# Kernel tuning notes

Measured on AMD Instinct MI355X. Metric: run time of the kernel, lower is better.

The kernel has to match this reference:

```python
import jax, jax.numpy as jnp
import numpy as np

B, S, K, E, H = 64, 25, 20, 256, 8
D = 2 * E  # MHA embed dim (item emb concat user emb)


def setup_inputs() -> dict:
    key = jax.random.key(0)
    ks = jax.random.split(key, 10)
    def w(k, shp, scale=0.02):
        return jax.random.normal(k, shp, jnp.float32) * scale
    return dict(
        item_embs=jax.random.normal(ks[0], (B, S, K, E), jnp.float32),
        user_embs=jax.random.normal(ks[1], (B, E), jnp.float32),
        responses=jax.random.randint(ks[2], (B, S, K), 0, 2),
        Wq=w(ks[3], (D, D)), bq=jnp.zeros((D,), jnp.float32),
        Wk=w(ks[4], (D, D)), bk=jnp.zeros((D,), jnp.float32),
        Wv=w(ks[5], (D, D)), bv=jnp.zeros((D,), jnp.float32),
        Wo=w(ks[6], (D, D)), bo=jnp.zeros((D,), jnp.float32),
        ln_g=jnp.ones((D,), jnp.float32), ln_b=jnp.zeros((D,), jnp.float32),
        W1=w(ks[7], (D, D)), b1=jnp.zeros((D,), jnp.float32),
        W2=w(ks[8], (1, D)), b2=jnp.zeros((1,), jnp.float32),
    )


def _scot_forward(item_embs, user_embs, responses, Wq, bq, Wk, bk, Wv, bv,
                  Wo, bo, ln_g, ln_b, W1, b1, W2, b2):
    Bt, St, Kt, Et = item_embs.shape
    Dt = 2 * Et
    L = St * Kt + 1  # all slate items + prepended zero item
    hd = Dt // H
    # stack_embeddings: concat item emb with broadcast user emb -> [B,S,K,2E]
    x = jnp.concatenate(
        [item_embs, jnp.broadcast_to(user_embs[:, None, None, :], (Bt, St, Kt, Et))], -1)
    x = x.reshape(Bt, St * Kt, Dt)
    # add_zero_item: prepend an all-zero token (slate number 0)
    x = jnp.concatenate([jnp.zeros((Bt, 1, Dt), x.dtype), x], axis=1)  # [B,L,D]
    # slate number per token: 0 for zero item, then 1..S repeated slate_size times
    slateno = jnp.concatenate(
        [jnp.zeros((1,), jnp.int32),
         jnp.repeat(jnp.arange(1, St + 1, dtype=jnp.int32), Kt)])  # [L]
    # clicked mask (zero item counts as clicked) -> keys visible to attention
    clicked = jnp.concatenate(
        [jnp.ones((Bt, 1), bool), responses.reshape(Bt, St * Kt) > 0], axis=1)  # [B,L]
    # attn_mask in the original blocks slateno_q <= slateno_k, except column 0;
    # combined with key_padding over non-clicked keys this equals:
    base_allow = slateno[:, None] > slateno[None, :]
    base_allow = base_allow.at[:, 0].set(True)            # zero item always visible
    allow = base_allow[None, :, :] & clicked[:, None, :]  # [B,L,L]
    # torch MultiheadAttention (batch_first)
    def heads(h):
        return h.reshape(Bt, L, H, hd).transpose(0, 2, 1, 3)  # [B,H,L,hd]
    q = heads(x @ Wq.T + bq)
    k = heads(x @ Wk.T + bk)
    v = heads(x @ Wv.T + bv)
    scores = jnp.einsum('bhqd,bhkd->bhqk', q, k) / np.sqrt(hd).astype(np.float32)
    scores = jnp.where(allow[:, None, :, :], scores, -jnp.inf)
    attn = jax.nn.softmax(scores, axis=-1)
    f = jnp.einsum('bhqk,bhkd->bhqd', attn, v)
    f = f.transpose(0, 2, 1, 3).reshape(Bt, L, Dt) @ Wo.T + bo
    f = f[:, 1:, :]  # drop zero-item query
    # out head: LayerNorm -> Linear -> GELU(exact) -> Linear
    mu = f.mean(-1, keepdims=True)
    var = ((f - mu) ** 2).mean(-1, keepdims=True)
    f = (f - mu) / jnp.sqrt(var + 1e-5) * ln_g + ln_b
    h = jax.nn.gelu(f @ W1.T + b1, approximate=False)
    out = h @ W2.T + b2  # [B, S*K, 1]
    return out.reshape(Bt, St, Kt)


def reference(item_embs, user_embs, responses, Wq, bq, Wk, bk, Wv, bv,
              Wo, bo, ln_g, ln_b, W1, b1, W2, b2):
    return _scot_forward(item_embs, user_embs, responses, Wq, bq, Wk, bk,
                         Wv, bv, Wo, bo, ln_g, ln_b, W1, b1, W2, b2)
```

## Files before the change

### kernel.cpp

```cpp
#include <hip/hip_runtime.h>
#include <math.h>

#define BATCH 64
#define SLATES 25
#define KPS 20
#define EDIM 256
#define DDIM 512
#define HEADS 8
#define HD 64
#define LFULL 501
#define NROWS 500
#define MTOT (BATCH*NROWS)
#define CMAX 512
#define NQKV 1536
#define RB 32
#define NRB ((NROWS + RB - 1) / RB)

typedef __attribute__((ext_vector_type(8))) short short8;
typedef __attribute__((ext_vector_type(4))) float f32x4;

__device__ __forceinline__ unsigned short f2bf(float x) {
    unsigned int u = __builtin_bit_cast(unsigned int, x);
    u = (u + 0x7FFFu + ((u >> 16) & 1u)) >> 16;
    return (unsigned short)u;
}
__device__ __forceinline__ float bf2f(unsigned short s) {
    unsigned int u = ((unsigned int)s) << 16;
    return __builtin_bit_cast(float, u);
}
__device__ __forceinline__ float gelu_exact(float x) {
    return 0.5f * x * (1.0f + erff(x * 0.70710678118654752440f));
}
__device__ __forceinline__ void gload16(const void* g, void* l) {
    __builtin_amdgcn_global_load_lds(
        (const __attribute__((address_space(1))) void*)g,
        (__attribute__((address_space(3))) void*)l, 16, 0, 0);
}

__global__ __launch_bounds__(256) void cvt_kernel(
    const float* __restrict__ src, unsigned short* __restrict__ dst, int n4)
{
    const int i = blockIdx.x * 256 + threadIdx.x;
    if (i >= n4) return;
    float4 v = ((const float4*)src)[i];
    ushort4 o;
    o.x = f2bf(v.x); o.y = f2bf(v.y); o.z = f2bf(v.z); o.w = f2bf(v.w);
    ((ushort4*)dst)[i] = o;
}

__global__ __launch_bounds__(256) void packqkv_kernel(
    const float* __restrict__ Wq, const float* __restrict__ Wk,
    const float* __restrict__ Wv, unsigned short* __restrict__ dst)
{
    const int y = blockIdx.y;
    const float* W = (y == 0) ? Wq : (y == 1) ? Wk : Wv;
    const int i = blockIdx.x * 256 + threadIdx.x;
    const int row = i >> 6, c4 = (i & 63) * 4;
    float4 v = *(const float4*)&W[(size_t)row * DDIM + c4];
    ushort4 o;
    o.x = f2bf(v.x); o.y = f2bf(v.y); o.z = f2bf(v.z); o.w = f2bf(v.w);
    *(ushort4*)&dst[((size_t)y * DDIM + row) * EDIM + c4] = o;
}

__global__ __launch_bounds__(256) void w1prep_kernel(
    const float* __restrict__ W1, const float* __restrict__ g,
    const float* __restrict__ lnb, unsigned short* __restrict__ W1g,
    float2* __restrict__ c1c2)
{
    const int row = blockIdx.x * 4 + (threadIdx.x >> 6);
    const int lane = threadIdx.x & 63;
    float c1 = 0.f, c2 = 0.f;
#pragma unroll
    for (int i = 0; i < 8; ++i) {
        const int k = lane + i * 64;
        const float w = W1[(size_t)row * DDIM + k];
        const float gv = g[k];
        c1 += w * lnb[k];
        c2 += w * gv;
        W1g[(size_t)row * DDIM + k] = f2bf(w * gv);
    }
#pragma unroll
    for (int off = 32; off; off >>= 1) {
        c1 += __shfl_xor(c1, off, 64);
        c2 += __shfl_xor(c2, off, 64);
    }
    if (lane == 0) c1c2[row] = make_float2(c1, c2);
}

__global__ __launch_bounds__(64) void compact_kernel(
    const int* __restrict__ resp, int* __restrict__ cidx, int* __restrict__ cnt)
{
    const int b = blockIdx.x, lane = threadIdx.x;
    int a[8]; int c = 0;
#pragma unroll
    for (int j = 0; j < 8; ++j) {
        const int l = lane * 8 + j;
        int al = 0;
        if (l == 0) al = 1;
        else if (l <= NROWS) al = (resp[(size_t)b * NROWS + l - 1] > 0) ? 1 : 0;
        a[j] = al; c += al;
    }
    int incl = c;
#pragma unroll
    for (int off = 1; off < 64; off <<= 1) {
        int t = __shfl_up(incl, off, 64);
        if (lane >= off) incl += t;
    }
    int run = incl - c;
#pragma unroll
    for (int j = 0; j < 8; ++j) {
        const int l = lane * 8 + j;
        if (l >= 1 && l <= 481 && (l % 20) == 1)
            cnt[b * 32 + (l - 1) / 20] = run;
        cidx[b * 512 + l] = a[j] ? run : -1;
        run += a[j];
    }
}

__global__ __launch_bounds__(256) void user_bias_kernel(
    const float* __restrict__ user,
    const float* __restrict__ Wq, const float* __restrict__ bq,
    const float* __restrict__ Wk, const float* __restrict__ bk,
    const float* __restrict__ Wv, const float* __restrict__ bv,
    float* __restrict__ uball,
    unsigned short* __restrict__ qb, unsigned short* __restrict__ kc,
    unsigned short* __restrict__ vc)
{
    const int b = blockIdx.x;
    const int y = blockIdx.y;
    const int tid = threadIdx.x;
    const float* W  = (y == 0) ? Wq : (y == 1) ? Wk : Wv;
    const float* bi = (y == 0) ? bq : (y == 1) ? bk : bv;

    __shared__ float us[EDIM];
    if (tid < EDIM) us[tid] = user[b * EDIM + tid];
    __syncthreads();
    for (int o = tid; o < DDIM; o += 256) {
        float s = bi[o];
        const float* wr = &W[(size_t)o * DDIM + EDIM];
#pragma unroll 4
        for (int e = 0; e < EDIM; ++e) s += us[e] * wr[e];
        uball[(size_t)b * NQKV + y * DDIM + o] = s;
        const int hh = o >> 6, dd = o & 63;
        const size_t bh = (size_t)b * HEADS + hh;
        if (y == 0)      qb[(bh * LFULL) * HD + dd] = f2bf(bi[o]);
        else if (y == 1) kc[(bh * CMAX) * HD + dd] = f2bf(bi[o]);
        else             vc[(bh * HD + dd) * CMAX] = f2bf(bi[o]);
    }
}

__global__ __launch_bounds__(256) void gemm_qkv(
    const unsigned short* __restrict__ A,
    const unsigned short* __restrict__ Wqkv,
    const float* __restrict__ uball, const int* __restrict__ cidx,
    unsigned short* __restrict__ oq, unsigned short* __restrict__ ok,
    unsigned short* __restrict__ ov)
{
    const int tid = threadIdx.x;
    const int lin = blockIdx.y * gridDim.x + blockIdx.x;
    const int vb  = (lin & 7) * 375 + (lin >> 3);
    const int n0 = (vb % 12) * 128;
    const int m0 = (vb / 12) * 128;
    const int lane = tid & 63, wid = tid >> 6;
    const int wm = (wid & 1) * 64, wn = (wid >> 1) * 64;

    __shared__ __align__(16) unsigned short sm[24576];
    __shared__ int cids[128];
    auto As = [&](int buf) { return (unsigned short(*)[32])(sm + buf * 4096); };
    auto Ws = [&](int buf) { return (unsigned short(*)[32])(sm + 12288 + buf * 4096); };
    auto bounce = (unsigned short(*)[136])sm;

    f32x4 acc[4][4];
#pragma unroll
    for (int i = 0; i < 4; ++i)
#pragma unroll
        for (int j = 0; j < 4; ++j) acc[i][j] = (f32x4){0.f, 0.f, 0.f, 0.f};

    const unsigned short* gA0 = &A[(size_t)(m0 + wid * 16 + (lane >> 2)) * EDIM + (lane & 3) * 8];
    const unsigned short* gA1 = gA0 + (size_t)64 * EDIM;
    const unsigned short* gW0 = &Wqkv[(size_t)(n0 + wid * 16 + (lane >> 2)) * EDIM + (lane & 3) * 8];
    const unsigned short* gW1 = gW0 + (size_t)64 * EDIM;
    const int frow = lane & 15, fk = (lane >> 4) * 8;

    auto stage = [&](int buf, int k0) {
        gload16(gA0 + k0, &As(buf)[wid * 16][0]);
        gload16(gA1 + k0, &As(buf)[64 + wid * 16][0]);
        gload16(gW0 + k0, &Ws(buf)[wid * 16][0]);
        gload16(gW1 + k0, &Ws(buf)[64 + wid * 16][0]);
    };
    stage(0, 0);
    stage(1, 32);

    const int nst = EDIM / 32;
    for (int t = 0; t < nst; ++t) {
        const int cur = t % 3;
        if (t < nst - 1) asm volatile("s_waitcnt vmcnt(4)" ::: "memory");
        else             asm volatile("s_waitcnt vmcnt(0)" ::: "memory");
        __builtin_amdgcn_s_barrier();
        __builtin_amdgcn_sched_barrier(0);
        short8 af[4], wf[4];
#pragma unroll
        for (int mi = 0; mi < 4; ++mi)
            af[mi] = *(const short8*)&As(cur)[wm + mi * 16 + frow][fk];
#pragma unroll
        for (int ni = 0; ni < 4; ++ni)
            wf[ni] = *(const short8*)&Ws(cur)[wn + ni * 16 + frow][fk];
#pragma unroll
        for (int mi = 0; mi < 4; ++mi)
#pragma unroll
            for (int ni = 0; ni < 4; ++ni)
                acc[mi][ni] = __builtin_amdgcn_mfma_f32_16x16x32_bf16(
                    af[mi], wf[ni], acc[mi][ni], 0, 0, 0);
        if (t + 2 < nst) stage((t + 2) % 3, (t + 2) * 32);
    }

    const int z = n0 >> 9;
    const int b0 = m0 / NROWS;
    const int split = (b0 + 1) * NROWS;
    const int b1 = (split <= m0 + 127) ? b0 + 1 : b0;
    float ub0[4], ub1[4];
#pragma unroll
    for (int ni = 0; ni < 4; ++ni) {
        const int np = n0 + wn + ni * 16 + frow;
        ub0[ni] = uball[(size_t)b0 * NQKV + np];
        ub1[ni] = uball[(size_t)b1 * NQKV + np];
    }
    __syncthreads();
    if (z != 0 && tid < 128) {
        const int m = m0 + tid;
        const int b = (m >= split) ? b1 : b0;
        cids[tid] = cidx[b * 512 + (m - b * NROWS + 1)];
    }
#pragma unroll
    for (int mi = 0; mi < 4; ++mi)
#pragma unroll
        for (int r = 0; r < 4; ++r) {
            const int ml = wm + mi * 16 + (lane >> 4) * 4 + r;
            const bool hi = (m0 + ml >= split);
#pragma unroll
            for (int ni = 0; ni < 4; ++ni)
                bounce[ml][wn + ni * 16 + frow] =
                    f2bf(acc[mi][ni][r] + (hi ? ub1[ni] : ub0[ni]));
        }
    __syncthreads();

    const int h0 = (n0 & 511) >> 6;
    if (z == 0) {
        const int row = tid >> 1, half = tid & 1;
        const int m = m0 + row;
        const int b = (m >= split) ? b1 : b0;
        const int l = m - b * NROWS + 1;
        unsigned short* dst = &oq[(((size_t)b * HEADS + h0 + half) * LFULL + l) * HD];
        const unsigned short* src = &bounce[row][half * 64];
#pragma unroll
        for (int j = 0; j < 8; ++j)
            *(uint4*)(dst + j * 8) = *(const uint4*)(src + j * 8);
    } else if (z == 1) {
        const int row = tid >> 1, half = tid & 1;
        const int c = cids[row];
        if (c >= 0) {
            const int m = m0 + row;
            const int b = (m >= split) ? b1 : b0;
            unsigned short* dst = &ok[(((size_t)b * HEADS + h0 + half) * CMAX + c) * HD];
            const unsigned short* src = &bounce[row][half * 64];
#pragma unroll
            for (int j = 0; j < 8; ++j)
                *(uint4*)(dst + j * 8) = *(const uint4*)(src + j * 8);
        }
    } else {
        const int col = tid & 127, mh = tid >> 7;
        const int hh = h0 + (col >> 6), dd = col & 63;
        for (int mm = 0; mm < 64; ++mm) {
            const int row = mh * 64 + mm;
            const int c = cids[row];
            if (c >= 0) {
                const int m = m0 + row;
                const int b = (m >= split) ? b1 : b0;
                ov[((size_t)b * HEADS + hh) * (size_t)(HD * CMAX)
                   + (size_t)dd * CMAX + c] = bounce[row][col];
            }
        }
    }
}

template <int MODE>
__global__ __launch_bounds__(256) void gemm_bf16(
    const unsigned short* __restrict__ A,
    const unsigned short* __restrict__ W,
    const float* __restrict__ bias, void* __restrict__ outp,
    const float* __restrict__ W2, float* __restrict__ part,
    const float2* __restrict__ musr, const float2* __restrict__ c1c2)
{
    const int tid = threadIdx.x;
    const int lin = blockIdx.y * gridDim.x + blockIdx.x;
    const int vb  = (lin & 7) * 125 + (lin >> 3);
    const int n0 = (vb % 4) * 128;
    const int m0 = (vb / 4) * 128;
    const int lane = tid & 63, wid = tid >> 6;
    const int wm = (wid & 1) * 64, wn = (wid >> 1) * 64;

    __shared__ unsigned short As[3][128][32];
    __shared__ unsigned short Ws[3][128][32];

    f32x4 acc[4][4];
#pragma unroll
    for (int i = 0; i < 4; ++i)
#pragma unroll
        for (int j = 0; j < 4; ++j) acc[i][j] = (f32x4){0.f, 0.f, 0.f, 0.f};

    const unsigned short* gA0 = &A[(size_t)(m0 + wid * 16 + (lane >> 2)) * DDIM + (lane & 3) * 8];
    const unsigned short* gA1 = gA0 + (size_t)64 * DDIM;
    const unsigned short* gW0 = &W[(size_t)(n0 + wid * 16 + (lane >> 2)) * DDIM + (lane & 3) * 8];
    const unsigned short* gW1 = gW0 + (size_t)64 * DDIM;
    const int frow = lane & 15, fk = (lane >> 4) * 8;

    auto stage = [&](int buf, int k0) {
        gload16(gA0 + k0, &As[buf][wid * 16][0]);
        gload16(gA1 + k0, &As[buf][64 + wid * 16][0]);
        gload16(gW0 + k0, &Ws[buf][wid * 16][0]);
        gload16(gW1 + k0, &Ws[buf][64 + wid * 16][0]);
    };
    stage(0, 0);
    stage(1, 32);

    const int nst = DDIM / 32;
    for (int t = 0; t < nst; ++t) {
        const int cur = t % 3;
        if (t < nst - 1) asm volatile("s_waitcnt vmcnt(4)" ::: "memory");
        else             asm volatile("s_waitcnt vmcnt(0)" ::: "memory");
        __builtin_amdgcn_s_barrier();
        __builtin_amdgcn_sched_barrier(0);
        short8 af[4], wf[4];
#pragma unroll
        for (int mi = 0; mi < 4; ++mi)
            af[mi] = *(const short8*)&As[cur][wm + mi * 16 + frow][fk];
#pragma unroll
        for (int ni = 0; ni < 4; ++ni)
            wf[ni] = *(const short8*)&Ws[cur][wn + ni * 16 + frow][fk];
#pragma unroll
        for (int mi = 0; mi < 4; ++mi)
#pragma unroll
            for (int ni = 0; ni < 4; ++ni)
                acc[mi][ni] = __builtin_amdgcn_mfma_f32_16x16x32_bf16(
                    af[mi], wf[ni], acc[mi][ni], 0, 0, 0);
        if (t + 2 < nst) stage((t + 2) % 3, (t + 2) * 32);
    }

    const int slot = (n0 >> 7) * 2 + (wn >> 6);
    if (MODE == 1) {
        float bv4[4];
#pragma unroll
        for (int ni = 0; ni < 4; ++ni) bv4[ni] = bias[n0 + wn + ni * 16 + frow];
#pragma unroll
        for (int mi = 0; mi < 4; ++mi)
#pragma unroll
            for (int r = 0; r < 4; ++r) {
                const int m = m0 + wm + mi * 16 + (lane >> 4) * 4 + r;
                float s1 = 0.f, s2 = 0.f;
#pragma unroll
                for (int ni = 0; ni < 4; ++ni) {
                    const float v = acc[mi][ni][r] + bv4[ni];
                    s1 += v; s2 += v * v;
                    ((unsigned short*)outp)[(size_t)m * DDIM + n0 + wn + ni * 16 + frow]
                        = f2bf(v);
                }
                s1 += __shfl_xor(s1, 1, 64); s2 += __shfl_xor(s2, 1, 64);
                s1 += __shfl_xor(s1, 2, 64); s2 += __shfl_xor(s2, 2, 64);
                s1 += __shfl_xor(s1, 4, 64); s2 += __shfl_xor(s2, 4, 64);
                s1 += __shfl_xor(s1, 8, 64); s2 += __shfl_xor(s2, 8, 64);
                if (frow == 0) {
                    part[((size_t)m << 4) + slot * 2]     = s1;
                    part[((size_t)m << 4) + slot * 2 + 1] = s2;
                }
            }
    } else {
        float w2v[4], cb[4], c2v[4];
#pragma unroll
        for (int ni = 0; ni < 4; ++ni) {
            const int n = n0 + wn + ni * 16 + frow;
            w2v[ni] = W2[n];
            const float2 cc = c1c2[n];
            cb[ni]  = cc.x + bias[n];
            c2v[ni] = cc.y;
        }
#pragma unroll
        for (int mi = 0; mi < 4; ++mi)
#pragma unroll
            for (int r = 0; r < 4; ++r) {
                const int m = m0 + wm + mi * 16 + (lane >> 4) * 4 + r;
                const float2 ms = musr[m];
                float s = 0.f;
#pragma unroll
                for (int ni = 0; ni < 4; ++ni)
                    s += gelu_exact(ms.y * (acc[mi][ni][r] - ms.x * c2v[ni]) + cb[ni])
                         * w2v[ni];
                s += __shfl_xor(s, 1, 64);
                s += __shfl_xor(s, 2, 64);
                s += __shfl_xor(s, 4, 64);
                s += __shfl_xor(s, 8, 64);
                if (frow == 0)
                    part[(size_t)m * 8 + slot] = s;
            }
    }
}

__global__ __launch_bounds__(256) void lnstats_kernel(
    const float* __restrict__ rowpart, float2* __restrict__ musr)
{
    const int m = blockIdx.x * 256 + threadIdx.x;
    if (m >= MTOT) return;
    const float* p = rowpart + ((size_t)m << 4);
    float s1 = 0.f, s2 = 0.f;
#pragma unroll
    for (int i = 0; i < 8; ++i) { s1 += p[i * 2]; s2 += p[i * 2 + 1]; }
    const float mu = s1 * (1.0f / DDIM);
    const float var = s2 * (1.0f / DDIM) - mu * mu;
    musr[m] = make_float2(mu, rsqrtf(var + 1e-5f));
}

__global__ __launch_bounds__(256) void w2red_kernel(
    const float* __restrict__ part, const float* __restrict__ b2,
    float* __restrict__ out)
{
    const int m = blockIdx.x * 256 + threadIdx.x;
    if (m >= MTOT) return;
    const float* p = part + (size_t)m * 8;
    float s = b2[0];
#pragma unroll
    for (int i = 0; i < 8; ++i) s += p[i];
    out[m] = s;
}

__global__ __launch_bounds__(256) void attn_mfma(
    const unsigned short* __restrict__ qx, const unsigned short* __restrict__ kc,
    const unsigned short* __restrict__ vc, const int* __restrict__ cnt,
    unsigned short* __restrict__ outb)
{
    const int lin = blockIdx.x + NRB * (blockIdx.y + HEADS * blockIdx.z);
    const int vbk = (lin & 7) * (NRB * HEADS * BATCH / 8) + (lin >> 3);
    const int rbk = vbk % NRB;
    const int h   = (vbk / NRB) % HEADS;
    const int b   = vbk / (NRB * HEADS);
    const int g0  = rbk * RB;

    const int tid = threadIdx.x, lane = tid & 63, w = tid >> 6;

    __shared__ __align__(16) unsigned short scb[RB][520];
    __shared__ float rsw[4][RB];
    __shared__ int snck[RB];

    const int frow = lane & 15, fk = (lane >> 4) * 8;
    const size_t bh = (size_t)b * HEADS + h;
    const unsigned short* kbase = kc + bh * (CMAX * HD);
    const unsigned short* vbase = vc + bh * (HD * CMAX);

    if (tid < RB) {
        const int s = (g0 + tid >= NROWS ? NROWS - 1 : g0 + tid) / KPS;
        snck[tid] = cnt[b * 32 + s];
    }

    short8 qf[2][2];
#pragma unroll
    for (int mi = 0; mi < 2; ++mi) {
        const int qrow = g0 + mi * 16 + frow;
#pragma unroll
        for (int ks = 0; ks < 2; ++ks) {
            short8 v = {};
            if (qrow < NROWS)
                v = *(const short8*)&qx[(bh * LFULL + qrow + 1) * HD + ks * 32 + fk];
            qf[mi][ks] = v;
        }
    }
    __syncthreads();

    int nck8[2][4];
#pragma unroll
    for (int mi = 0; mi < 2; ++mi)
#pragma unroll
        for (int r = 0; r < 4; ++r)
            nck8[mi][r] = snck[mi * 16 + (lane >> 4) * 4 + r];
    const int nmax = snck[RB - 1];
    const int NT = (nmax + 63) >> 6;

    f32x4 rsum[2];
    rsum[0] = (f32x4){0.f, 0.f, 0.f, 0.f};
    rsum[1] = (f32x4){0.f, 0.f, 0.f, 0.f};
    for (int t = 0; t < NT; ++t) {
        const int key = (t << 6) + w * 16 + frow;
        const unsigned short* kr = kbase + (size_t)key * HD;
        const short8 kf0 = *(const short8*)(kr + fk);
        const short8 kf1 = *(const short8*)(kr + 32 + fk);
        f32x4 s2[2];
#pragma unroll
        for (int mi = 0; mi < 2; ++mi) {
            s2[mi] = (f32x4){0.f, 0.f, 0.f, 0.f};
            s2[mi] = __builtin_amdgcn_mfma_f32_16x16x32_bf16(qf[mi][0], kf0, s2[mi], 0, 0, 0);
            s2[mi] = __builtin_amdgcn_mfma_f32_16x16x32_bf16(qf[mi][1], kf1, s2[mi], 0, 0, 0);
        }
#pragma unroll
        for (int mi = 0; mi < 2; ++mi)
#pragma unroll
            for (int r = 0; r < 4; ++r) {
                const int row = mi * 16 + (lane >> 4) * 4 + r;
                const float p = (key < nck8[mi][r]) ? __expf(s2[mi][r] * 0.125f) : 0.f;
                rsum[mi][r] += p;
                scb[row][key] = f2bf(p);
            }
    }
#pragma unroll
    for (int mi = 0; mi < 2; ++mi)
#pragma unroll
        for (int r = 0; r < 4; ++r) {
            float v = rsum[mi][r];
            v += __shfl_xor(v, 1, 64);
            v += __shfl_xor(v, 2, 64);
            v += __shfl_xor(v, 4, 64);
            v += __shfl_xor(v, 8, 64);
            if (frow == 0)
                rsw[w][mi * 16 + (lane >> 4) * 4 + r] = v;
        }
    __syncthreads();

    f32x4 po[2];
    po[0] = (f32x4){0.f, 0.f, 0.f, 0.f};
    po[1] = (f32x4){0.f, 0.f, 0.f, 0.f};
    const unsigned short* vrow = vbase + (size_t)(w * 16 + frow) * CMAX;
    for (int t = 0; t < NT; ++t) {
#pragma unroll
        for (int ks = 0; ks < 2; ++ks) {
            const int kb0 = (t << 6) + ks * 32 + fk;
            const short8 vf = *(const short8*)(vrow + kb0);
#pragma unroll
            for (int mi = 0; mi < 2; ++mi) {
                const short8 pf = *(const short8*)&scb[mi * 16 + frow][kb0];
                po[mi] = __builtin_amdgcn_mfma_f32_16x16x32_bf16(pf, vf, po[mi], 0, 0, 0);
            }
        }
    }

#pragma unroll
    for (int mi = 0; mi < 2; ++mi)
#pragma unroll
        for (int r = 0; r < 4; ++r) {
            const int row = mi * 16 + (lane >> 4) * 4 + r;
            const int m = g0 + row;
            if (m < NROWS) {
                const float inv = 1.0f / (rsw[0][row] + rsw[1][row]
                                        + rsw[2][row] + rsw[3][row]);
                outb[((size_t)b * NROWS + m) * DDIM
                     + h * HD + w * 16 + frow] = f2bf(po[mi][r] * inv);
            }
        }
}

extern "C" void kernel_launch(void* const* d_in, const int* in_sizes, int n_in,
                              void* d_out, int out_size, void* d_ws, size_t ws_size,
                              hipStream_t stream)
{
    const float* item = (const float*)d_in[0];
    const float* user = (const float*)d_in[1];
    const int*   resp = (const int*)d_in[2];
    const float* Wq = (const float*)d_in[3];  const float* bq = (const float*)d_in[4];
    const float* Wk = (const float*)d_in[5];  const float* bk = (const float*)d_in[6];
    const float* Wv = (const float*)d_in[7];  const float* bv = (const float*)d_in[8];
    const float* Wo = (const float*)d_in[9];  const float* bo = (const float*)d_in[10];
    const float* lng = (const float*)d_in[11]; const float* lnb = (const float*)d_in[12];
    const float* W1 = (const float*)d_in[13]; const float* b1 = (const float*)d_in[14];
    const float* W2 = (const float*)d_in[15]; const float* b2 = (const float*)d_in[16];
    float* out = (float*)d_out;

    char* p = (char*)d_ws;
    auto alloc = [&](size_t bytes) { char* r = p; p += (bytes + 255) & ~(size_t)255; return r; };
    const size_t NITEM = (size_t)BATCH * NROWS * EDIM;
    const size_t NW    = (size_t)DDIM * DDIM;
    const size_t NQ    = (size_t)BATCH * HEADS * LFULL * HD;
    const size_t NC    = (size_t)BATCH * HEADS * CMAX * HD;
    const size_t NMD   = (size_t)MTOT * DDIM;
    const size_t PAD   = 8192;

    unsigned short* itemb  = (unsigned short*)alloc(NITEM * 2);
    unsigned short* Wqkvb  = (unsigned short*)alloc((size_t)NQKV * EDIM * 2);
    unsigned short* Wob    = (unsigned short*)alloc(NW * 2);
    unsigned short* W1gb   = (unsigned short*)alloc(NW * 2);
    unsigned short* qb     = (unsigned short*)alloc(NQ * 2 + PAD);
    unsigned short* kcb    = (unsigned short*)alloc(NC * 2 + PAD);
    unsigned short* vcb    = (unsigned short*)alloc(NC * 2 + PAD);
    unsigned short* aob    = (unsigned short*)alloc(NMD * 2);
    unsigned short* fb16   = (unsigned short*)alloc(NMD * 2);
    float*  uball  = (float*)alloc((size_t)BATCH * NQKV * 4);
    float*  part   = (float*)alloc((size_t)MTOT * 8 * 4);
    float*  rowpart= (float*)alloc((size_t)MTOT * 16 * 4);
    float2* musr   = (float2*)alloc((size_t)MTOT * 8);
    float2* c1c2   = (float2*)alloc((size_t)DDIM * 8);
    int* cidx    = (int*)alloc((size_t)BATCH * 512 * 4);
    int* cnt     = (int*)alloc((size_t)BATCH * 32 * 4);

    cvt_kernel<<<dim3((NITEM / 4 + 255) / 256), 256, 0, stream>>>(item, itemb, NITEM / 4);
    packqkv_kernel<<<dim3(DDIM * EDIM / 4 / 256, 3), 256, 0, stream>>>(Wq, Wk, Wv, Wqkvb);
    cvt_kernel<<<dim3(NW / 4 / 256), 256, 0, stream>>>(Wo, Wob, NW / 4);
    w1prep_kernel<<<dim3(DDIM / 4), 256, 0, stream>>>(W1, lng, lnb, W1gb, c1c2);

    compact_kernel<<<dim3(BATCH), 64, 0, stream>>>(resp, cidx, cnt);

    user_bias_kernel<<<dim3(BATCH, 3), 256, 0, stream>>>(
        user, Wq, bq, Wk, bk, Wv, bv, uball, qb, kcb, vcb);

    gemm_qkv<<<dim3(NQKV / 128, MTOT / 128), 256, 0, stream>>>(
        itemb, Wqkvb, uball, cidx, qb, kcb, vcb);

    attn_mfma<<<dim3(NRB, HEADS, BATCH), 256, 0, stream>>>(qb, kcb, vcb, cnt, aob);

    dim3 gg(DDIM / 128, MTOT / 128);
    gemm_bf16<1><<<gg, 256, 0, stream>>>(aob, Wob, bo, fb16, nullptr, rowpart,
                                         nullptr, nullptr);
    lnstats_kernel<<<dim3((MTOT + 255) / 256), 256, 0, stream>>>(rowpart, musr);
    gemm_bf16<2><<<gg, 256, 0, stream>>>(fb16, W1gb, b1, nullptr, W2, part,
                                         musr, c1c2);
    w2red_kernel<<<dim3((MTOT + 255) / 256), 256, 0, stream>>>(part, b2, out);
}
```

Baseline: 257.5 us.

## Switch GEMM k-loop from triple to double buffered LDS pipeline

Both GEMM kernels move from a 3-stage LDS ring with prefetch distance 2 to 2-stage double buffering. Each iteration now issues the next stage's loads before its MFMAs, then waits and barriers at the end. This cuts LDS use, which could let more blocks fit per CU, and shrinks the QKV bounce padding. The cost is only one stage of latency hiding plus a full vmcnt(0) wait every iteration.

```diff
diff --git a/kernel.cpp b/kernel.cpp
--- a/kernel.cpp
+++ b/kernel.cpp
@@ -15,6 +15,7 @@
 #define NQKV 1536
 #define RB 32
 #define NRB ((NROWS + RB - 1) / RB)
+#define BPAD 134
 
 typedef __attribute__((ext_vector_type(8))) short short8;
 typedef __attribute__((ext_vector_type(4))) float f32x4;
@@ -164,11 +165,11 @@
     const int lane = tid & 63, wid = tid >> 6;
     const int wm = (wid & 1) * 64, wn = (wid >> 1) * 64;
 
-    __shared__ __align__(16) unsigned short sm[24576];
+    __shared__ __align__(16) unsigned short sm[128 * BPAD];
     __shared__ int cids[128];
     auto As = [&](int buf) { return (unsigned short(*)[32])(sm + buf * 4096); };
-    auto Ws = [&](int buf) { return (unsigned short(*)[32])(sm + 12288 + buf * 4096); };
-    auto bounce = (unsigned short(*)[136])sm;
+    auto Ws = [&](int buf) { return (unsigned short(*)[32])(sm + 8192 + buf * 4096); };
+    auto bounce = (unsigned short(*)[BPAD])sm;
 
     f32x4 acc[4][4];
 #pragma unroll
@@ -189,15 +190,14 @@
         gload16(gW1 + k0, &Ws(buf)[64 + wid * 16][0]);
     };
     stage(0, 0);
-    stage(1, 32);
+    asm volatile("s_waitcnt vmcnt(0)" ::: "memory");
+    __builtin_amdgcn_s_barrier();
+    __builtin_amdgcn_sched_barrier(0);
 
     const int nst = EDIM / 32;
+    int cur = 0;
     for (int t = 0; t < nst; ++t) {
-        const int cur = t % 3;
-        if (t < nst - 1) asm volatile("s_waitcnt vmcnt(4)" ::: "memory");
-        else             asm volatile("s_waitcnt vmcnt(0)" ::: "memory");
-        __builtin_amdgcn_s_barrier();
-        __builtin_amdgcn_sched_barrier(0);
+        if (t + 1 < nst) stage(cur ^ 1, (t + 1) * 32);
         short8 af[4], wf[4];
 #pragma unroll
         for (int mi = 0; mi < 4; ++mi)
@@ -211,7 +211,10 @@
             for (int ni = 0; ni < 4; ++ni)
                 acc[mi][ni] = __builtin_amdgcn_mfma_f32_16x16x32_bf16(
                     af[mi], wf[ni], acc[mi][ni], 0, 0, 0);
-        if (t + 2 < nst) stage((t + 2) % 3, (t + 2) * 32);
+        asm volatile("s_waitcnt vmcnt(0)" ::: "memory");
+        __builtin_amdgcn_s_barrier();
+        __builtin_amdgcn_sched_barrier(0);
+        cur ^= 1;
     }
 
     const int z = n0 >> 9;
@@ -225,7 +228,6 @@
         ub0[ni] = uball[(size_t)b0 * NQKV + np];
         ub1[ni] = uball[(size_t)b1 * NQKV + np];
     }
-    __syncthreads();
     if (z != 0 && tid < 128) {
         const int m = m0 + tid;
         const int b = (m >= split) ? b1 : b0;
@@ -299,8 +301,8 @@
     const int lane = tid & 63, wid = tid >> 6;
     const int wm = (wid & 1) * 64, wn = (wid >> 1) * 64;
 
-    __shared__ unsigned short As[3][128][32];
-    __shared__ unsigned short Ws[3][128][32];
+    __shared__ unsigned short As[2][128][32];
+    __shared__ unsigned short Ws[2][128][32];
 
     f32x4 acc[4][4];
 #pragma unroll
@@ -321,15 +323,14 @@
         gload16(gW1 + k0, &Ws[buf][64 + wid * 16][0]);
     };
     stage(0, 0);
-    stage(1, 32);
+    asm volatile("s_waitcnt vmcnt(0)" ::: "memory");
+    __builtin_amdgcn_s_barrier();
+    __builtin_amdgcn_sched_barrier(0);
 
     const int nst = DDIM / 32;
+    int cur = 0;
     for (int t = 0; t < nst; ++t) {
-        const int cur = t % 3;
-        if (t < nst - 1) asm volatile("s_waitcnt vmcnt(4)" ::: "memory");
-        else             asm volatile("s_waitcnt vmcnt(0)" ::: "memory");
-        __builtin_amdgcn_s_barrier();
-        __builtin_amdgcn_sched_barrier(0);
+        if (t + 1 < nst) stage(cur ^ 1, (t + 1) * 32);
         short8 af[4], wf[4];
 #pragma unroll
         for (int mi = 0; mi < 4; ++mi)
@@ -343,7 +344,10 @@
             for (int ni = 0; ni < 4; ++ni)
                 acc[mi][ni] = __builtin_amdgcn_mfma_f32_16x16x32_bf16(
                     af[mi], wf[ni], acc[mi][ni], 0, 0, 0);
-        if (t + 2 < nst) stage((t + 2) % 3, (t + 2) * 32);
+        asm volatile("s_waitcnt vmcnt(0)" ::: "memory");
+        __builtin_amdgcn_s_barrier();
+        __builtin_amdgcn_sched_barrier(0);
+        cur ^= 1;
     }
 
     const int slot = (n0 >> 7) * 2 + (wn >> 6);
```

New measurement: 271.4 us. 1.05x slower.
